# Optimization experiments

Measured on AMD Instinct MI355X. Metric: run time of the kernel, lower is better.

The kernel has to match this reference:

```python
import jax, jax.numpy as jnp
import numpy as np

B, S, E = 2048, 23, 768
RED, H, NUM_LABELS = 256, 8, 25
DH = RED // H
DELTA = 0.1
EPS_LN = 1e-5


def setup_inputs() -> dict:
    key = jax.random.key(0)
    ks = jax.random.split(key, 20)
    g = lambda k, shape, fan: jax.random.normal(k, shape, dtype=jnp.float32) * (1.0 / np.sqrt(fan))
    inp = {
        'cls_embeddings': jax.random.normal(ks[0], (B, S, E), dtype=jnp.float32),
        'existing_mask': jax.random.randint(ks[1], (B, S), 0, 2, dtype=jnp.int32),
        'missing_emb': g(ks[2], (S, E), E),
        'W1': g(ks[3], (E // 2, E), E), 'b1': jnp.zeros((E // 2,), jnp.float32),
        'W2': g(ks[4], (RED, E // 2), E // 2), 'b2': jnp.zeros((RED,), jnp.float32),
        'ln_g': jnp.ones((RED,), jnp.float32), 'ln_b': jnp.zeros((RED,), jnp.float32),
        'Wq': g(ks[5], (RED, RED), RED), 'bq': jnp.zeros((RED,), jnp.float32),
        'Wk': g(ks[6], (RED, RED), RED), 'bk': jnp.zeros((RED,), jnp.float32),
        'Wv': g(ks[7], (RED, RED), RED), 'bv': jnp.zeros((RED,), jnp.float32),
        'Wo': g(ks[8], (RED, RED), RED), 'bo': jnp.zeros((RED,), jnp.float32),
        'Wp': g(ks[9], (NUM_LABELS, RED), RED), 'bp': jnp.zeros((NUM_LABELS,), jnp.float32),
    }
    return inp


def _layer_norm(x, g, b):
    mu = jnp.mean(x, axis=-1, keepdims=True)
    var = jnp.mean(jnp.square(x - mu), axis=-1, keepdims=True)
    return (x - mu) * jax.lax.rsqrt(var + EPS_LN) * g + b


def _forward(cls_embeddings, existing_mask, missing_emb, W1, b1, W2, b2, ln_g, ln_b,
             Wq, bq, Wk, bk, Wv, bv, Wo, bo, Wp, bp):
    exist = existing_mask > 0                              # [B,S] bool
    # Gather: existing sections use BERT CLS, missing slots use learned embeddings
    sec = jnp.where(exist[..., None], cls_embeddings, missing_emb[None])  # [B,S,E]
    # SectionDimReducer (exact-erf GELU as in nn.GELU default)
    h = jax.nn.gelu(sec @ W1.T + b1, approximate=False)
    h = jax.nn.gelu(h @ W2.T + b2, approximate=False)
    red = _layer_norm(h, ln_g, ln_b)                       # [B,S,RED]
    # Tiny MHA: every slot queries the existing sections of its own EHR
    q = (red @ Wq.T + bq).reshape(B, S, H, DH)
    k = (red @ Wk.T + bk).reshape(B, S, H, DH)
    v = (red @ Wv.T + bv).reshape(B, S, H, DH)
    scores = jnp.einsum('bqhd,bkhd->bhqk', q, k) / np.sqrt(DH)
    scores = jnp.where(exist[:, None, None, :], scores, -1e9)
    attn = jax.nn.softmax(scores, axis=-1)                 # [B,H,S,S]
    ctx = jnp.einsum('bhqk,bkhd->bqhd', attn, v).reshape(B, S, RED)
    mha_out = ctx @ Wo.T + bo                              # [B,S,RED]
    # Scatter: only missing slots (of EHRs with >=1 existing section) are replaced
    any_exist = jnp.any(exist, axis=1)                     # [B]
    use_attn = (~exist) & any_exist[:, None]               # [B,S]
    updated = jnp.where(use_attn[..., None], mha_out, red)
    # margin-based orthogonality loss on section embeddings
    norm = updated / jnp.maximum(jnp.linalg.norm(updated, axis=-1, keepdims=True), 1e-8)
    gram = jnp.einsum('bid,bjd->bij', norm, norm)          # [B,S,S]
    off = 1.0 - jnp.eye(S, dtype=updated.dtype)
    loss_orth = jnp.sum(jax.nn.relu(jnp.abs(gram) - DELTA) * off) / (B * S * (S - 1))
    logits = updated.mean(axis=1) @ Wp.T + bp              # [B,NUM_LABELS]
    return loss_orth, logits


def reference(cls_embeddings, existing_mask, missing_emb, W1, b1, W2, b2, ln_g, ln_b,
              Wq, bq, Wk, bk, Wv, bv, Wo, bo, Wp, bp):
    return _forward(cls_embeddings, existing_mask, missing_emb, W1, b1, W2, b2, ln_g, ln_b,
                    Wq, bq, Wk, bk, Wv, bv, Wo, bo, Wp, bp)
```

## Files before the change

kernel.cpp:

```cpp
#include <hip/hip_runtime.h>

typedef unsigned short u16;
typedef unsigned int u32;
typedef __attribute__((ext_vector_type(8))) short short8;
typedef __attribute__((ext_vector_type(4))) float f32x4;

struct __align__(8) us4 { u16 x, y, z, w; };

__device__ __forceinline__ float bf1(u16 v){ return __uint_as_float(((u32)v) << 16); }
__device__ __forceinline__ float bflo(u32 u){ return __uint_as_float(u << 16); }
__device__ __forceinline__ float bfhi(u32 u){ return __uint_as_float(u & 0xFFFF0000u); }
__device__ __forceinline__ u16 fbf(float f){
    u32 u = __float_as_uint(f);
    return (u16)((u + 0x7FFFu + ((u >> 16) & 1u)) >> 16);
}
__device__ __forceinline__ float gelu_exact(float x){
    return 0.5f * x * (1.0f + erff(x * 0.70710678118654752f));
}
__device__ __forceinline__ void unp8(uint4 u, float* f){
    f[0]=bflo(u.x); f[1]=bfhi(u.x); f[2]=bflo(u.y); f[3]=bfhi(u.y);
    f[4]=bflo(u.z); f[5]=bfhi(u.z); f[6]=bflo(u.w); f[7]=bfhi(u.w);
}
__device__ __forceinline__ uint4 pack8(float4 a, float4 b){
    uint4 u;
    u.x = (u32)fbf(a.x) | ((u32)fbf(a.y) << 16);
    u.y = (u32)fbf(a.z) | ((u32)fbf(a.w) << 16);
    u.z = (u32)fbf(b.x) | ((u32)fbf(b.y) << 16);
    u.w = (u32)fbf(b.z) | ((u32)fbf(b.w) << 16);
    return u;
}

#define MFMA16(a, b, c) __builtin_amdgcn_mfma_f32_16x16x32_bf16(a, b, c, 0, 0, 0)
#define QSTR 264


__global__ __launch_bounds__(256) void wconv(
    const float* __restrict__ W1, const float* __restrict__ W2,
    const float* __restrict__ Wq, const float* __restrict__ Wk,
    const float* __restrict__ Wv, const float* __restrict__ Wo,
    const float* __restrict__ Wp, u16* __restrict__ dst)
{
    const int i = blockIdx.x * 256 + threadIdx.x;
    const float* s; int o;
    if      (i < 294912) { s = W1; o = i; }
    else if (i < 393216) { s = W2; o = i - 294912; }
    else if (i < 458752) { s = Wq; o = i - 393216; }
    else if (i < 524288) { s = Wk; o = i - 458752; }
    else if (i < 589824) { s = Wv; o = i - 524288; }
    else if (i < 655360) { s = Wo; o = i - 589824; }
    else                 { s = Wp; o = i - 655360; }
    dst[i] = fbf(s[o]);
}

__global__ __launch_bounds__(256) void gemm1_kernel(
    const float* __restrict__ cls, const int* __restrict__ mask,
    const float* __restrict__ missing, const u16* __restrict__ W,
    const float* __restrict__ bias, u16* __restrict__ C)
{
    const int K = 768, M = 384;
    __shared__ u16 As[128 * 40];
    __shared__ u16 Bs[128 * 40];
    const int tid = threadIdx.x;
    const int w = tid >> 6, lane = tid & 63;
    const int nBase = blockIdx.y * 128, mBase = blockIdx.x * 128;
    const int wr = w >> 1, wc = w & 1;
    const int r0 = tid >> 2;
    const int co = (tid & 3) * 8;
    const int frow = lane & 15, quad = lane >> 4;

    const int rowA0 = nBase + r0, rowA1 = nBase + r0 + 64;
    const float* ap0 = (mask[rowA0] > 0) ? cls + (size_t)rowA0 * 768
                                         : missing + (size_t)(rowA0 % 23) * 768;
    const float* ap1 = (mask[rowA1] > 0) ? cls + (size_t)rowA1 * 768
                                         : missing + (size_t)(rowA1 % 23) * 768;
    const u16* bp0 = W + (size_t)(mBase + r0) * K;
    const u16* bp1 = W + (size_t)(mBase + r0 + 64) * K;

    f32x4 acc[4][4];
#pragma unroll
    for (int mt = 0; mt < 4; ++mt)
#pragma unroll
        for (int nt = 0; nt < 4; ++nt) acc[mt][nt] = f32x4{0.f, 0.f, 0.f, 0.f};

    float4 a0a = *(const float4*)(ap0 + co), a0b = *(const float4*)(ap0 + co + 4);
    float4 a1a = *(const float4*)(ap1 + co), a1b = *(const float4*)(ap1 + co + 4);
    uint4 pb0 = *(const uint4*)(bp0 + co), pb1 = *(const uint4*)(bp1 + co);

    for (int k0 = 0; k0 < K; k0 += 32) {
        __syncthreads();
        *(uint4*)(As + r0 * 40 + co) = pack8(a0a, a0b);
        *(uint4*)(As + (r0 + 64) * 40 + co) = pack8(a1a, a1b);
        *(uint4*)(Bs + r0 * 40 + co) = pb0;
        *(uint4*)(Bs + (r0 + 64) * 40 + co) = pb1;
        __syncthreads();
        if (k0 + 32 < K) {
            const int kn = k0 + 32 + co;
            a0a = *(const float4*)(ap0 + kn); a0b = *(const float4*)(ap0 + kn + 4);
            a1a = *(const float4*)(ap1 + kn); a1b = *(const float4*)(ap1 + kn + 4);
            pb0 = *(const uint4*)(bp0 + kn);  pb1 = *(const uint4*)(bp1 + kn);
        }
        short8 af[4], bfv[4];
#pragma unroll
        for (int mt = 0; mt < 4; ++mt)
            af[mt] = *(const short8*)(As + (wr * 64 + mt * 16 + frow) * 40 + quad * 8);
#pragma unroll
        for (int nt = 0; nt < 4; ++nt)
            bfv[nt] = *(const short8*)(Bs + (wc * 64 + nt * 16 + frow) * 40 + quad * 8);
#pragma unroll
        for (int mt = 0; mt < 4; ++mt)
#pragma unroll
            for (int nt = 0; nt < 4; ++nt)
                acc[mt][nt] = MFMA16(af[mt], bfv[nt], acc[mt][nt]);
    }

#pragma unroll
    for (int nt = 0; nt < 4; ++nt) {
        const int col = mBase + wc * 64 + nt * 16 + frow;
        const float bv = bias[col];
#pragma unroll
        for (int mt = 0; mt < 4; ++mt)
#pragma unroll
            for (int reg = 0; reg < 4; ++reg) {
                const int row = nBase + wr * 64 + mt * 16 + quad * 4 + reg;
                C[(size_t)row * M + col] = fbf(gelu_exact(acc[mt][nt][reg] + bv));
            }
    }
}

__global__ __launch_bounds__(256) void gemm_bt(
    const u16* __restrict__ A, const u16* __restrict__ W,
    const float* __restrict__ bias, u16* __restrict__ C, int K, int M)
{
    __shared__ u16 As[128 * 40];
    __shared__ u16 Bs[128 * 40];
    const int tid = threadIdx.x;
    const int w = tid >> 6, lane = tid & 63;
    const int nBase = blockIdx.y * 128, mBase = blockIdx.x * 128;
    const int wr = w >> 1, wc = w & 1;
    const int r0 = tid >> 2;
    const int co = (tid & 3) * 8;
    const int frow = lane & 15, quad = lane >> 4;

    f32x4 acc[4][4];
#pragma unroll
    for (int mt = 0; mt < 4; ++mt)
#pragma unroll
        for (int nt = 0; nt < 4; ++nt) acc[mt][nt] = f32x4{0.f, 0.f, 0.f, 0.f};

    uint4 pa0 = *(const uint4*)(A + (size_t)(nBase + r0) * K + co);
    uint4 pa1 = *(const uint4*)(A + (size_t)(nBase + r0 + 64) * K + co);
    uint4 pb0 = *(const uint4*)(W + (size_t)(mBase + r0) * K + co);
    uint4 pb1 = *(const uint4*)(W + (size_t)(mBase + r0 + 64) * K + co);

    for (int k0 = 0; k0 < K; k0 += 32) {
        __syncthreads();
        *(uint4*)(As + r0 * 40 + co) = pa0;
        *(uint4*)(As + (r0 + 64) * 40 + co) = pa1;
        *(uint4*)(Bs + r0 * 40 + co) = pb0;
        *(uint4*)(Bs + (r0 + 64) * 40 + co) = pb1;
        __syncthreads();
        if (k0 + 32 < K) {
            const int kn = k0 + 32 + co;
            pa0 = *(const uint4*)(A + (size_t)(nBase + r0) * K + kn);
            pa1 = *(const uint4*)(A + (size_t)(nBase + r0 + 64) * K + kn);
            pb0 = *(const uint4*)(W + (size_t)(mBase + r0) * K + kn);
            pb1 = *(const uint4*)(W + (size_t)(mBase + r0 + 64) * K + kn);
        }
        short8 af[4], bfv[4];
#pragma unroll
        for (int mt = 0; mt < 4; ++mt)
            af[mt] = *(const short8*)(As + (wr * 64 + mt * 16 + frow) * 40 + quad * 8);
#pragma unroll
        for (int nt = 0; nt < 4; ++nt)
            bfv[nt] = *(const short8*)(Bs + (wc * 64 + nt * 16 + frow) * 40 + quad * 8);
#pragma unroll
        for (int mt = 0; mt < 4; ++mt)
#pragma unroll
            for (int nt = 0; nt < 4; ++nt)
                acc[mt][nt] = MFMA16(af[mt], bfv[nt], acc[mt][nt]);
    }

#pragma unroll
    for (int nt = 0; nt < 4; ++nt) {
        const int col = mBase + wc * 64 + nt * 16 + frow;
        const float bv = bias[col];
#pragma unroll
        for (int mt = 0; mt < 4; ++mt)
#pragma unroll
            for (int reg = 0; reg < 4; ++reg) {
                const int row = nBase + wr * 64 + mt * 16 + quad * 4 + reg;
                C[(size_t)row * M + col] = fbf(gelu_exact(acc[mt][nt][reg] + bv));
            }
    }
}

__device__ __forceinline__ void ln_rows_inplace(
    u16* base, int t, const float* __restrict__ lng, const float* __restrict__ lnb)
{
    const int r = t >> 3, sub = t & 7;
    if (r >= 23) return;
    u16* rp = base + r * QSTR + sub * 32;
    float x[32];
    unp8(((const uint4*)rp)[0], x);
    unp8(((const uint4*)rp)[1], x + 8);
    unp8(((const uint4*)rp)[2], x + 16);
    unp8(((const uint4*)rp)[3], x + 24);
    float s = 0.f;
#pragma unroll
    for (int e = 0; e < 32; ++e) s += x[e];
    s += __shfl_xor(s, 1); s += __shfl_xor(s, 2); s += __shfl_xor(s, 4);
    const float mu = s * (1.f / 256.f);
    float vs = 0.f;
#pragma unroll
    for (int e = 0; e < 32; ++e) { const float d = x[e] - mu; vs += d * d; }
    vs += __shfl_xor(vs, 1); vs += __shfl_xor(vs, 2); vs += __shfl_xor(vs, 4);
    const float rs = rsqrtf(vs * (1.f / 256.f) + 1e-5f);
#pragma unroll
    for (int c8 = 0; c8 < 4; ++c8) {
        const int cb = sub * 32 + c8 * 8;
        const float4 g0 = *(const float4*)(lng + cb), g1 = *(const float4*)(lng + cb + 4);
        const float4 b0 = *(const float4*)(lnb + cb), b1 = *(const float4*)(lnb + cb + 4);
        float4 ya, yb;
        ya.x = (x[c8*8+0]-mu)*rs*g0.x + b0.x;
        ya.y = (x[c8*8+1]-mu)*rs*g0.y + b0.y;
        ya.z = (x[c8*8+2]-mu)*rs*g0.z + b0.z;
        ya.w = (x[c8*8+3]-mu)*rs*g0.w + b0.w;
        yb.x = (x[c8*8+4]-mu)*rs*g1.x + b1.x;
        yb.y = (x[c8*8+5]-mu)*rs*g1.y + b1.y;
        yb.z = (x[c8*8+6]-mu)*rs*g1.z + b1.z;
        yb.w = (x[c8*8+7]-mu)*rs*g1.w + b1.w;
        ((uint4*)rp)[c8] = pack8(ya, yb);
    }
}

__global__ __launch_bounds__(256) void attn_tail_kernel(
    const u16* __restrict__ redb, const int* __restrict__ mask,
    const u16* __restrict__ Wqkvb,
    const float* __restrict__ bq, const float* __restrict__ bk,
    const float* __restrict__ bv, const u16* __restrict__ Wob,
    const float* __restrict__ bo, const float* __restrict__ lng,
    const float* __restrict__ lnb, const u16* __restrict__ Wpb,
    const float* __restrict__ bp, float* __restrict__ out,
    float* __restrict__ lossAcc)
{
    __shared__ __align__(16) unsigned char SM[40960];
    u16* s_rq = (u16*)SM;
    u16* s_k  = (u16*)(SM + 12144);
    u16* s_vT = (u16*)(SM + 24288);
    int* sEx   = (int*)(SM + 40672);
    int* sMiss = (int*)(SM + 40764);
    float* sDiag = (float*)(SM + 24288);
    float* sInv  = (float*)(SM + 24384);
    float* sPool = (float*)(SM + 24480);

    const int b = blockIdx.x, t = threadIdx.x;
    const int w = t >> 6, lane = t & 63;
    const int frow = lane & 15, quad = lane >> 4;
    const int r0c = frow;
    const int r1c = (16 + frow > 22) ? 22 : 16 + frow;
    const f32x4 z4 = f32x4{0.f, 0.f, 0.f, 0.f};

    {
        const int myEx = (t < 23) ? mask[b * 23 + t] : 0;
        if (t < 23) sEx[t] = myEx;
        if (t < 64) {
            const unsigned long long ball = __ballot((t < 23) && (myEx > 0));
            if (t < 23) sMiss[t] = (ball != 0ull && myEx <= 0) ? 1 : 0;
        }
    }
    for (int i = t; i < 1024; i += 256) ((uint4*)s_vT)[i] = make_uint4(0u, 0u, 0u, 0u);
    for (int i = t; i < 736; i += 256) {
        const int s = i >> 5, c8 = (i & 31) * 8;
        *(uint4*)(s_rq + s * QSTR + c8) =
            *(const uint4*)(redb + ((size_t)(b * 23 + s)) * 256 + c8);
    }
    __syncthreads();

    ln_rows_inplace(s_rq, t, lng, lnb);
    __syncthreads();

#define QKV_KLOOP(SEGBASE, ACC)                                                   \
    for (int k0 = 0; k0 < 256; k0 += 32) {                                        \
        short8 a0 = *(const short8*)(s_rq + r0c * QSTR + k0 + quad * 8);          \
        short8 a1 = *(const short8*)(s_rq + r1c * QSTR + k0 + quad * 8);          \
        _Pragma("unroll")                                                         \
        for (int nt = 0; nt < 4; ++nt) {                                          \
            const int n = (SEGBASE) + w * 64 + nt * 16 + frow;                    \
            short8 bfr = *(const short8*)(Wqkvb + (size_t)n * 256 + k0 + quad * 8); \
            ACC[0][nt] = MFMA16(a0, bfr, ACC[0][nt]);                             \
            ACC[1][nt] = MFMA16(a1, bfr, ACC[1][nt]);                             \
        }                                                                         \
    }

    {
        f32x4 ka[2][4];
#pragma unroll
        for (int mt = 0; mt < 2; ++mt)
#pragma unroll
            for (int nt = 0; nt < 4; ++nt) ka[mt][nt] = z4;
        QKV_KLOOP(256, ka)
#pragma unroll
        for (int nt = 0; nt < 4; ++nt) {
            const int cm = w * 64 + nt * 16 + frow;
            const float bb = bk[cm];
#pragma unroll
            for (int mt = 0; mt < 2; ++mt)
#pragma unroll
                for (int reg = 0; reg < 4; ++reg) {
                    const int s = mt * 16 + quad * 4 + reg;
                    if (s < 23) s_k[s * QSTR + cm] = fbf(ka[mt][nt][reg] + bb);
                }
        }
    }
    {
        f32x4 va[2][4];
#pragma unroll
        for (int mt = 0; mt < 2; ++mt)
#pragma unroll
            for (int nt = 0; nt < 4; ++nt) va[mt][nt] = z4;
        QKV_KLOOP(512, va)
#pragma unroll
        for (int nt = 0; nt < 4; ++nt) {
            const int cm = w * 64 + nt * 16 + frow;
            const float bb = bv[cm];
#pragma unroll
            for (int mt = 0; mt < 2; ++mt)
#pragma unroll
                for (int reg = 0; reg < 4; ++reg) {
                    const int s = mt * 16 + quad * 4 + reg;
                    if (s < 23) s_vT[cm * 32 + s] = fbf(va[mt][nt][reg] + bb);
                }
        }
    }
    {
        f32x4 qa[2][4];
#pragma unroll
        for (int mt = 0; mt < 2; ++mt)
#pragma unroll
            for (int nt = 0; nt < 4; ++nt) qa[mt][nt] = z4;
        QKV_KLOOP(0, qa)
        __syncthreads();
#pragma unroll
        for (int nt = 0; nt < 4; ++nt) {
            const int cm = w * 64 + nt * 16 + frow;
            const float bb = bq[cm];
#pragma unroll
            for (int mt = 0; mt < 2; ++mt)
#pragma unroll
                for (int reg = 0; reg < 4; ++reg) {
                    const int s = mt * 16 + quad * 4 + reg;
                    if (s < 23) s_rq[s * QSTR + cm] = fbf(qa[mt][nt][reg] + bb);
                }
        }
    }

    {
        const float scl = 0.17677669529663687f;
        const float m0 = (sEx[frow] > 0) ? 0.f : -1e9f;
        const float m1 = (16 + frow < 23 && sEx[16 + frow] > 0) ? 0.f : -1e9f;
#pragma unroll
        for (int hh2 = 0; hh2 < 2; ++hh2) {
            const int hb = w * 64 + hh2 * 32;
            short8 aq0 = *(const short8*)(s_rq + r0c * QSTR + hb + quad * 8);
            short8 aq1 = *(const short8*)(s_rq + r1c * QSTR + hb + quad * 8);
            short8 bk0 = *(const short8*)(s_k + r0c * QSTR + hb + quad * 8);
            short8 bk1 = *(const short8*)(s_k + r1c * QSTR + hb + quad * 8);
            f32x4 s00 = MFMA16(aq0, bk0, z4);
            f32x4 s01 = MFMA16(aq0, bk1, z4);
            f32x4 s10 = MFMA16(aq1, bk0, z4);
            f32x4 s11 = MFMA16(aq1, bk1, z4);
#pragma unroll
            for (int mt = 0; mt < 2; ++mt) {
                f32x4& c0 = mt ? s10 : s00;
                f32x4& c1 = mt ? s11 : s01;
#pragma unroll
                for (int reg = 0; reg < 4; ++reg) {
                    float v0 = c0[reg] * scl + m0;
                    float v1 = c1[reg] * scl + m1;
                    float mx = fmaxf(v0, v1);
#pragma unroll
                    for (int m = 8; m; m >>= 1) mx = fmaxf(mx, __shfl_xor(mx, m));
                    float p0 = __expf(v0 - mx), p1 = __expf(v1 - mx);
                    float sm = p0 + p1;
#pragma unroll
                    for (int m = 8; m; m >>= 1) sm += __shfl_xor(sm, m);
                    const float inv = 1.f / sm;
                    c0[reg] = p0 * inv;
                    c1[reg] = p1 * inv;
                }
            }
#pragma unroll
            for (int reg = 0; reg < 4; ++reg) {
                const int q0r = quad * 4 + reg;
                s_k[q0r * QSTR + hb + frow]      = fbf(s00[reg]);
                s_k[q0r * QSTR + hb + 16 + frow] = fbf(s01[reg]);
                const int q1r = 16 + quad * 4 + reg;
                if (q1r < 23) {
                    s_k[q1r * QSTR + hb + frow]      = fbf(s10[reg]);
                    s_k[q1r * QSTR + hb + 16 + frow] = fbf(s11[reg]);
                }
            }
            short8 pa0 = *(const short8*)(s_k + r0c * QSTR + hb + quad * 8);
            short8 pa1 = *(const short8*)(s_k + r1c * QSTR + hb + quad * 8);
            short8 bv0 = *(const short8*)(s_vT + (hb + frow) * 32 + quad * 8);
            short8 bv1 = *(const short8*)(s_vT + (hb + 16 + frow) * 32 + quad * 8);
            f32x4 c00 = MFMA16(pa0, bv0, z4);
            f32x4 c01 = MFMA16(pa0, bv1, z4);
            f32x4 c10 = MFMA16(pa1, bv0, z4);
            f32x4 c11 = MFMA16(pa1, bv1, z4);
#pragma unroll
            for (int reg = 0; reg < 4; ++reg) {
                const int q0r = quad * 4 + reg;
                s_rq[q0r * QSTR + hb + frow]      = fbf(c00[reg]);
                s_rq[q0r * QSTR + hb + 16 + frow] = fbf(c01[reg]);
                const int q1r = 16 + quad * 4 + reg;
                if (q1r < 23) {
                    s_rq[q1r * QSTR + hb + frow]      = fbf(c10[reg]);
                    s_rq[q1r * QSTR + hb + 16 + frow] = fbf(c11[reg]);
                }
            }
        }
    }
    __syncthreads();

    {
        const u16* src = redb + (size_t)(b * 23) * 256;
        const int s0 = t >> 5, c0o = (t & 31) * 8;
        uint4 rg0 = *(const uint4*)(src + s0 * 256 + c0o);
        uint4 rg1 = *(const uint4*)(src + (s0 + 8) * 256 + c0o);
        uint4 rg2;
        const bool has2 = (t + 512) < 736;
        if (has2) rg2 = *(const uint4*)(src + (s0 + 16) * 256 + c0o);

        f32x4 wacc[2][4];
#pragma unroll
        for (int mt = 0; mt < 2; ++mt)
#pragma unroll
            for (int nt = 0; nt < 4; ++nt) wacc[mt][nt] = z4;
        for (int k0 = 0; k0 < 256; k0 += 32) {
            short8 a0 = *(const short8*)(s_rq + r0c * QSTR + k0 + quad * 8);
            short8 a1 = *(const short8*)(s_rq + r1c * QSTR + k0 + quad * 8);
#pragma unroll
            for (int nt = 0; nt < 4; ++nt) {
                const int n = w * 64 + nt * 16 + frow;
                short8 bfr = *(const short8*)(Wob + (size_t)n * 256 + k0 + quad * 8);
                wacc[0][nt] = MFMA16(a0, bfr, wacc[0][nt]);
                wacc[1][nt] = MFMA16(a1, bfr, wacc[1][nt]);
            }
        }
        *(uint4*)(s_k + s0 * QSTR + c0o) = rg0;
        *(uint4*)(s_k + (s0 + 8) * QSTR + c0o) = rg1;
        if (has2) *(uint4*)(s_k + (s0 + 16) * QSTR + c0o) = rg2;
        __syncthreads();
        ln_rows_inplace(s_k, t, lng, lnb);
        __syncthreads();
#pragma unroll
        for (int nt = 0; nt < 4; ++nt) {
            const int col = w * 64 + nt * 16 + frow;
            const float bvv = bo[col];
#pragma unroll
            for (int mt = 0; mt < 2; ++mt)
#pragma unroll
                for (int reg = 0; reg < 4; ++reg) {
                    const int s = mt * 16 + quad * 4 + reg;
                    if (s < 23 && sMiss[s])
                        s_k[s * QSTR + col] = fbf(wacc[mt][nt][reg] + bvv);
                }
        }
    }
    __syncthreads();

    f32x4 g00 = z4, g01 = z4, g10 = z4, g11 = z4;
    if (w == 0) {
        for (int k0 = 0; k0 < 256; k0 += 32) {
            short8 a0 = *(const short8*)(s_k + r0c * QSTR + k0 + quad * 8);
            short8 a1 = *(const short8*)(s_k + r1c * QSTR + k0 + quad * 8);
            g00 = MFMA16(a0, a0, g00);
            g01 = MFMA16(a0, a1, g01);
            g10 = MFMA16(a1, a0, g10);
            g11 = MFMA16(a1, a1, g11);
        }
#pragma unroll
        for (int reg = 0; reg < 4; ++reg) {
            if (frow == quad * 4 + reg) {
                sDiag[frow] = g00[reg];
                if (16 + frow < 23) sDiag[16 + frow] = g11[reg];
            }
        }
    } else {
        for (int c = t - 64; c < 256; c += 192) {
            float pv = 0.f;
#pragma unroll
            for (int s = 0; s < 23; ++s) pv += bf1(s_k[s * QSTR + c]);
            sPool[c] = pv * (1.f / 23.f);
        }
    }
    __syncthreads();
    if (t < 23) sInv[t] = 1.f / fmaxf(sqrtf(sDiag[t]), 1e-8f);
    __syncthreads();

    if (w == 0) {
        float contrib = 0.f;
        const float ic0 = sInv[frow];
        const float ic1 = (16 + frow < 23) ? sInv[16 + frow] : 0.f;
        const bool c1ok = (16 + frow < 23);
#pragma unroll
        for (int reg = 0; reg < 4; ++reg) {
            const int rA = quad * 4 + reg;
            const float irA = sInv[rA];
            if (rA != frow) {
                const float cc = fabsf(g00[reg] * irA * ic0) - 0.1f;
                if (cc > 0.f) contrib += cc;
            }
            if (c1ok) {
                const float cc = fabsf(g01[reg] * irA * ic1) - 0.1f;
                if (cc > 0.f) contrib += cc;
            }
            const int rB = 16 + quad * 4 + reg;
            if (rB < 23) {
                const float irB = sInv[rB];
                {
                    const float cc = fabsf(g10[reg] * irB * ic0) - 0.1f;
                    if (cc > 0.f) contrib += cc;
                }
                if (c1ok && rB != 16 + frow) {
                    const float cc = fabsf(g11[reg] * irB * ic1) - 0.1f;
                    if (cc > 0.f) contrib += cc;
                }
            }
        }
#pragma unroll
        for (int m = 32; m; m >>= 1) contrib += __shfl_xor(contrib, m);
        if (lane == 0) atomicAdd(lossAcc, contrib);
    } else {
        const int li = t - 64;
#pragma unroll 1
        for (int pass = 0; pass < 2; ++pass) {
            int L, chunk;
            if (pass == 0) { L = li >> 3; chunk = li & 7; }
            else { if (li >= 8) break; L = 24; chunk = li; }
            float a = 0.f;
#pragma unroll
            for (int q4 = 0; q4 < 4; ++q4) {
                const int c8 = chunk * 4 + q4;
                float wf[8]; unp8(*(const uint4*)(Wpb + (size_t)L * 256 + c8 * 8), wf);
                const float4 p0 = *(const float4*)(sPool + c8 * 8);
                const float4 p1 = *(const float4*)(sPool + c8 * 8 + 4);
                a += wf[0] * p0.x + wf[1] * p0.y + wf[2] * p0.z + wf[3] * p0.w
                   + wf[4] * p1.x + wf[5] * p1.y + wf[6] * p1.z + wf[7] * p1.w;
            }
            a += __shfl_xor(a, 1); a += __shfl_xor(a, 2); a += __shfl_xor(a, 4);
            if (chunk == 0) out[1 + b * 25 + L] = a + bp[L];
        }
    }
}

__global__ void loss_finalize(const float* __restrict__ lossAcc, float* __restrict__ out)
{
    out[0] = lossAcc[0] * (1.f / 1036288.f);
}

extern "C" void kernel_launch(void* const* d_in, const int* in_sizes, int n_in,
                              void* d_out, int out_size, void* d_ws, size_t ws_size,
                              hipStream_t stream)
{
    const float* cls     = (const float*)d_in[0];
    const int*   mask    = (const int*)d_in[1];
    const float* missing = (const float*)d_in[2];
    const float* W1 = (const float*)d_in[3];  const float* b1 = (const float*)d_in[4];
    const float* W2 = (const float*)d_in[5];  const float* b2 = (const float*)d_in[6];
    const float* lng = (const float*)d_in[7]; const float* lnb = (const float*)d_in[8];
    const float* Wq = (const float*)d_in[9];  const float* bq = (const float*)d_in[10];
    const float* Wk = (const float*)d_in[11]; const float* bk = (const float*)d_in[12];
    const float* Wv = (const float*)d_in[13]; const float* bv = (const float*)d_in[14];
    const float* Wo = (const float*)d_in[15]; const float* bo = (const float*)d_in[16];
    const float* Wp = (const float*)d_in[17]; const float* bp = (const float*)d_in[18];
    float* out = (float*)d_out;

    char* ws = (char*)d_ws;
    u16* h1b  = (u16*)ws;
    u16* redb = (u16*)(ws + 36175872);
    u16* Wb   = (u16*)(ws + 60293120);
    u16* W1b   = Wb;
    u16* W2b   = Wb + 294912;
    u16* Wqkvb = Wb + 393216;
    u16* Wob   = Wb + 589824;
    u16* Wpb   = Wb + 655360;
    float* lossAcc = (float*)(ws + 61616640);

    hipMemsetAsync(lossAcc, 0, sizeof(float), stream);

    wconv<<<2585, 256, 0, stream>>>(W1, W2, Wq, Wk, Wv, Wo, Wp, Wb);
    gemm1_kernel<<<dim3(3, 368), 256, 0, stream>>>(cls, mask, missing, W1b, b1, h1b);
    gemm_bt<<<dim3(2, 368), 256, 0, stream>>>(h1b, W2b, b2, redb, 384, 256);
    attn_tail_kernel<<<2048, 256, 0, stream>>>(redb, mask, Wqkvb, bq, bk, bv,
                                               Wob, bo, lng, lnb, Wpb, bp,
                                               out, lossAcc);
    loss_finalize<<<1, 1, 0, stream>>>(lossAcc, out);
}
```

Measured before the change: 550.5 us.

## Fuse layernorm into register loads and software-prefetch weight fragments in attention tail

The layernorm on the reduced rows is now applied in registers right after the global load and written to shared memory once, which removes a shared-memory round trip and a barrier, in both the initial and the residual paths. The QKV and output projection k-loops now use a macro that prefetches the next weight fragments while the current MFMAs run. The gram loop and the pooling weights for the classifier head are also prefetched early. Launch bounds now request 4 blocks per SM, which may force register spilling given the extra prefetch registers.

```diff
diff --git a/kernel.cpp b/kernel.cpp
--- a/kernel.cpp
+++ b/kernel.cpp
@@ -194,46 +194,71 @@
     }
 }
 
-__device__ __forceinline__ void ln_rows_inplace(
-    u16* base, int t, const float* __restrict__ lng, const float* __restrict__ lnb)
-{
-    const int r = t >> 3, sub = t & 7;
-    if (r >= 23) return;
-    u16* rp = base + r * QSTR + sub * 32;
-    float x[32];
-    unp8(((const uint4*)rp)[0], x);
-    unp8(((const uint4*)rp)[1], x + 8);
-    unp8(((const uint4*)rp)[2], x + 16);
-    unp8(((const uint4*)rp)[3], x + 24);
-    float s = 0.f;
-#pragma unroll
-    for (int e = 0; e < 32; ++e) s += x[e];
+__device__ __forceinline__ void ln1_reg(
+    const float* x, const float4& g0, const float4& g1,
+    const float4& b0, const float4& b1, u16* rp)
+{
+    float s = x[0] + x[1] + x[2] + x[3] + x[4] + x[5] + x[6] + x[7];
     s += __shfl_xor(s, 1); s += __shfl_xor(s, 2); s += __shfl_xor(s, 4);
+    s += __shfl_xor(s, 8); s += __shfl_xor(s, 16);
     const float mu = s * (1.f / 256.f);
-    float vs = 0.f;
-#pragma unroll
-    for (int e = 0; e < 32; ++e) { const float d = x[e] - mu; vs += d * d; }
-    vs += __shfl_xor(vs, 1); vs += __shfl_xor(vs, 2); vs += __shfl_xor(vs, 4);
-    const float rs = rsqrtf(vs * (1.f / 256.f) + 1e-5f);
-#pragma unroll
-    for (int c8 = 0; c8 < 4; ++c8) {
-        const int cb = sub * 32 + c8 * 8;
-        const float4 g0 = *(const float4*)(lng + cb), g1 = *(const float4*)(lng + cb + 4);
-        const float4 b0 = *(const float4*)(lnb + cb), b1 = *(const float4*)(lnb + cb + 4);
-        float4 ya, yb;
-        ya.x = (x[c8*8+0]-mu)*rs*g0.x + b0.x;
-        ya.y = (x[c8*8+1]-mu)*rs*g0.y + b0.y;
-        ya.z = (x[c8*8+2]-mu)*rs*g0.z + b0.z;
-        ya.w = (x[c8*8+3]-mu)*rs*g0.w + b0.w;
-        yb.x = (x[c8*8+4]-mu)*rs*g1.x + b1.x;
-        yb.y = (x[c8*8+5]-mu)*rs*g1.y + b1.y;
-        yb.z = (x[c8*8+6]-mu)*rs*g1.z + b1.z;
-        yb.w = (x[c8*8+7]-mu)*rs*g1.w + b1.w;
-        ((uint4*)rp)[c8] = pack8(ya, yb);
-    }
-}
-
-__global__ __launch_bounds__(256) void attn_tail_kernel(
+    float v = 0.f;
+#pragma unroll
+    for (int e = 0; e < 8; ++e) { const float d = x[e] - mu; v += d * d; }
+    v += __shfl_xor(v, 1); v += __shfl_xor(v, 2); v += __shfl_xor(v, 4);
+    v += __shfl_xor(v, 8); v += __shfl_xor(v, 16);
+    const float rs = rsqrtf(v * (1.f / 256.f) + 1e-5f);
+    float4 ya, yb;
+    ya.x = (x[0]-mu)*rs*g0.x + b0.x;
+    ya.y = (x[1]-mu)*rs*g0.y + b0.y;
+    ya.z = (x[2]-mu)*rs*g0.z + b0.z;
+    ya.w = (x[3]-mu)*rs*g0.w + b0.w;
+    yb.x = (x[4]-mu)*rs*g1.x + b1.x;
+    yb.y = (x[5]-mu)*rs*g1.y + b1.y;
+    yb.z = (x[6]-mu)*rs*g1.z + b1.z;
+    yb.w = (x[7]-mu)*rs*g1.w + b1.w;
+    *(uint4*)rp = pack8(ya, yb);
+}
+
+__device__ __forceinline__ void ln3_reg_store(
+    uint4 rg0, uint4 rg1, uint4 rg2, bool has2,
+    const float* __restrict__ lng, const float* __restrict__ lnb,
+    u16* dstBase, int s0, int c0o)
+{
+    const float4 g0 = *(const float4*)(lng + c0o);
+    const float4 g1 = *(const float4*)(lng + c0o + 4);
+    const float4 b0 = *(const float4*)(lnb + c0o);
+    const float4 b1 = *(const float4*)(lnb + c0o + 4);
+    float x[8];
+    unp8(rg0, x); ln1_reg(x, g0, g1, b0, b1, dstBase + s0 * QSTR + c0o);
+    unp8(rg1, x); ln1_reg(x, g0, g1, b0, b1, dstBase + (s0 + 8) * QSTR + c0o);
+    if (has2) { unp8(rg2, x); ln1_reg(x, g0, g1, b0, b1, dstBase + (s0 + 16) * QSTR + c0o); }
+}
+
+#define KLOOP_PF(WPTR, SRC, ACC)                                                  \
+    {                                                                             \
+        short8 nb0 = *(const short8*)(WPTR);                                      \
+        short8 nb1 = *(const short8*)((WPTR) + 16 * 256);                         \
+        short8 nb2 = *(const short8*)((WPTR) + 32 * 256);                         \
+        short8 nb3 = *(const short8*)((WPTR) + 48 * 256);                         \
+        for (int k0 = 0; k0 < 256; k0 += 32) {                                    \
+            short8 a0 = *(const short8*)((SRC) + r0c * QSTR + k0 + quad * 8);     \
+            short8 a1 = *(const short8*)((SRC) + r1c * QSTR + k0 + quad * 8);     \
+            short8 c0 = nb0, c1 = nb1, c2 = nb2, c3 = nb3;                        \
+            if (k0 + 32 < 256) {                                                  \
+                nb0 = *(const short8*)((WPTR) + (k0 + 32));                       \
+                nb1 = *(const short8*)((WPTR) + 16 * 256 + (k0 + 32));            \
+                nb2 = *(const short8*)((WPTR) + 32 * 256 + (k0 + 32));            \
+                nb3 = *(const short8*)((WPTR) + 48 * 256 + (k0 + 32));            \
+            }                                                                     \
+            ACC[0][0] = MFMA16(a0, c0, ACC[0][0]); ACC[1][0] = MFMA16(a1, c0, ACC[1][0]); \
+            ACC[0][1] = MFMA16(a0, c1, ACC[0][1]); ACC[1][1] = MFMA16(a1, c1, ACC[1][1]); \
+            ACC[0][2] = MFMA16(a0, c2, ACC[0][2]); ACC[1][2] = MFMA16(a1, c2, ACC[1][2]); \
+            ACC[0][3] = MFMA16(a0, c3, ACC[0][3]); ACC[1][3] = MFMA16(a1, c3, ACC[1][3]); \
+        }                                                                         \
+    }
+
+__global__ __launch_bounds__(256, 4) void attn_tail_kernel(
     const u16* __restrict__ redb, const int* __restrict__ mask,
     const u16* __restrict__ Wqkvb,
     const float* __restrict__ bq, const float* __restrict__ bk,
@@ -269,46 +294,38 @@
         }
     }
     for (int i = t; i < 1024; i += 256) ((uint4*)s_vT)[i] = make_uint4(0u, 0u, 0u, 0u);
-    for (int i = t; i < 736; i += 256) {
-        const int s = i >> 5, c8 = (i & 31) * 8;
-        *(uint4*)(s_rq + s * QSTR + c8) =
-            *(const uint4*)(redb + ((size_t)(b * 23 + s)) * 256 + c8);
+
+    {
+        const u16* src = redb + (size_t)(b * 23) * 256;
+        const int s0 = t >> 5, c0o = (t & 31) * 8;
+        uint4 rg0 = *(const uint4*)(src + s0 * 256 + c0o);
+        uint4 rg1 = *(const uint4*)(src + (s0 + 8) * 256 + c0o);
+        uint4 rg2 = make_uint4(0u, 0u, 0u, 0u);
+        const bool has2 = t < 224;
+        if (has2) rg2 = *(const uint4*)(src + (s0 + 16) * 256 + c0o);
+        ln3_reg_store(rg0, rg1, rg2, has2, lng, lnb, s_rq, s0, c0o);
     }
     __syncthreads();
 
-    ln_rows_inplace(s_rq, t, lng, lnb);
-    __syncthreads();
-
-#define QKV_KLOOP(SEGBASE, ACC)                                                   \
-    for (int k0 = 0; k0 < 256; k0 += 32) {                                        \
-        short8 a0 = *(const short8*)(s_rq + r0c * QSTR + k0 + quad * 8);          \
-        short8 a1 = *(const short8*)(s_rq + r1c * QSTR + k0 + quad * 8);          \
-        _Pragma("unroll")                                                         \
-        for (int nt = 0; nt < 4; ++nt) {                                          \
-            const int n = (SEGBASE) + w * 64 + nt * 16 + frow;                    \
-            short8 bfr = *(const short8*)(Wqkvb + (size_t)n * 256 + k0 + quad * 8); \
-            ACC[0][nt] = MFMA16(a0, bfr, ACC[0][nt]);                             \
-            ACC[1][nt] = MFMA16(a1, bfr, ACC[1][nt]);                             \
-        }                                                                         \
-    }
-
+    const int cmb = w * 64 + frow;
     {
         f32x4 ka[2][4];
 #pragma unroll
         for (int mt = 0; mt < 2; ++mt)
 #pragma unroll
             for (int nt = 0; nt < 4; ++nt) ka[mt][nt] = z4;
-        QKV_KLOOP(256, ka)
+        const u16* wp = Wqkvb + (size_t)(256 + cmb) * 256 + quad * 8;
+        const float bb[4] = {bk[cmb], bk[cmb + 16], bk[cmb + 32], bk[cmb + 48]};
+        KLOOP_PF(wp, s_rq, ka)
 #pragma unroll
         for (int nt = 0; nt < 4; ++nt) {
-            const int cm = w * 64 + nt * 16 + frow;
-            const float bb = bk[cm];
+            const int cm = cmb + nt * 16;
 #pragma unroll
             for (int mt = 0; mt < 2; ++mt)
 #pragma unroll
                 for (int reg = 0; reg < 4; ++reg) {
                     const int s = mt * 16 + quad * 4 + reg;
-                    if (s < 23) s_k[s * QSTR + cm] = fbf(ka[mt][nt][reg] + bb);
+                    if (s < 23) s_k[s * QSTR + cm] = fbf(ka[mt][nt][reg] + bb[nt]);
                 }
         }
     }
@@ -318,17 +335,18 @@
         for (int mt = 0; mt < 2; ++mt)
 #pragma unroll
             for (int nt = 0; nt < 4; ++nt) va[mt][nt] = z4;
-        QKV_KLOOP(512, va)
+        const u16* wp = Wqkvb + (size_t)(512 + cmb) * 256 + quad * 8;
+        const float bb[4] = {bv[cmb], bv[cmb + 16], bv[cmb + 32], bv[cmb + 48]};
+        KLOOP_PF(wp, s_rq, va)
 #pragma unroll
         for (int nt = 0; nt < 4; ++nt) {
-            const int cm = w * 64 + nt * 16 + frow;
-            const float bb = bv[cm];
+            const int cm = cmb + nt * 16;
 #pragma unroll
             for (int mt = 0; mt < 2; ++mt)
 #pragma unroll
                 for (int reg = 0; reg < 4; ++reg) {
                     const int s = mt * 16 + quad * 4 + reg;
-                    if (s < 23) s_vT[cm * 32 + s] = fbf(va[mt][nt][reg] + bb);
+                    if (s < 23) s_vT[cm * 32 + s] = fbf(va[mt][nt][reg] + bb[nt]);
                 }
         }
     }
@@ -338,18 +356,19 @@
         for (int mt = 0; mt < 2; ++mt)
 #pragma unroll
             for (int nt = 0; nt < 4; ++nt) qa[mt][nt] = z4;
-        QKV_KLOOP(0, qa)
+        const u16* wp = Wqkvb + (size_t)cmb * 256 + quad * 8;
+        const float bb[4] = {bq[cmb], bq[cmb + 16], bq[cmb + 32], bq[cmb + 48]};
+        KLOOP_PF(wp, s_rq, qa)
         __syncthreads();
 #pragma unroll
         for (int nt = 0; nt < 4; ++nt) {
-            const int cm = w * 64 + nt * 16 + frow;
-            const float bb = bq[cm];
+            const int cm = cmb + nt * 16;
 #pragma unroll
             for (int mt = 0; mt < 2; ++mt)
 #pragma unroll
                 for (int reg = 0; reg < 4; ++reg) {
                     const int s = mt * 16 + quad * 4 + reg;
-                    if (s < 23) s_rq[s * QSTR + cm] = fbf(qa[mt][nt][reg] + bb);
+                    if (s < 23) s_rq[s * QSTR + cm] = fbf(qa[mt][nt][reg] + bb[nt]);
                 }
         }
     }
@@ -428,8 +447,8 @@
         const int s0 = t >> 5, c0o = (t & 31) * 8;
         uint4 rg0 = *(const uint4*)(src + s0 * 256 + c0o);
         uint4 rg1 = *(const uint4*)(src + (s0 + 8) * 256 + c0o);
-        uint4 rg2;
-        const bool has2 = (t + 512) < 736;
+        uint4 rg2 = make_uint4(0u, 0u, 0u, 0u);
+        const bool has2 = t < 224;
         if (has2) rg2 = *(const uint4*)(src + (s0 + 16) * 256 + c0o);
 
         f32x4 wacc[2][4];
@@ -437,44 +456,38 @@
         for (int mt = 0; mt < 2; ++mt)
 #pragma unroll
             for (int nt = 0; nt < 4; ++nt) wacc[mt][nt] = z4;
-        for (int k0 = 0; k0 < 256; k0 += 32) {
-            short8 a0 = *(const short8*)(s_rq + r0c * QSTR + k0 + quad * 8);
-            short8 a1 = *(const short8*)(s_rq + r1c * QSTR + k0 + quad * 8);
-#pragma unroll
-            for (int nt = 0; nt < 4; ++nt) {
-                const int n = w * 64 + nt * 16 + frow;
-                short8 bfr = *(const short8*)(Wob + (size_t)n * 256 + k0 + quad * 8);
-                wacc[0][nt] = MFMA16(a0, bfr, wacc[0][nt]);
-                wacc[1][nt] = MFMA16(a1, bfr, wacc[1][nt]);
-            }
-        }
-        *(uint4*)(s_k + s0 * QSTR + c0o) = rg0;
-        *(uint4*)(s_k + (s0 + 8) * QSTR + c0o) = rg1;
-        if (has2) *(uint4*)(s_k + (s0 + 16) * QSTR + c0o) = rg2;
+        const u16* wp = Wob + (size_t)cmb * 256 + quad * 8;
+        const float ob[4] = {bo[cmb], bo[cmb + 16], bo[cmb + 32], bo[cmb + 48]};
+        KLOOP_PF(wp, s_rq, wacc)
+        ln3_reg_store(rg0, rg1, rg2, has2, lng, lnb, s_k, s0, c0o);
         __syncthreads();
-        ln_rows_inplace(s_k, t, lng, lnb);
-        __syncthreads();
 #pragma unroll
         for (int nt = 0; nt < 4; ++nt) {
-            const int col = w * 64 + nt * 16 + frow;
-            const float bvv = bo[col];
+            const int col = cmb + nt * 16;
 #pragma unroll
             for (int mt = 0; mt < 2; ++mt)
 #pragma unroll
                 for (int reg = 0; reg < 4; ++reg) {
                     const int s = mt * 16 + quad * 4 + reg;
                     if (s < 23 && sMiss[s])
-                        s_k[s * QSTR + col] = fbf(wacc[mt][nt][reg] + bvv);
+                        s_k[s * QSTR + col] = fbf(wacc[mt][nt][reg] + ob[nt]);
                 }
         }
     }
     __syncthreads();
 
     f32x4 g00 = z4, g01 = z4, g10 = z4, g11 = z4;
+    uint4 wpre[4];
+    int Lpre = 0, chpre = 0;
     if (w == 0) {
+        short8 ga0 = *(const short8*)(s_k + r0c * QSTR + quad * 8);
+        short8 ga1 = *(const short8*)(s_k + r1c * QSTR + quad * 8);
         for (int k0 = 0; k0 < 256; k0 += 32) {
-            short8 a0 = *(const short8*)(s_k + r0c * QSTR + k0 + quad * 8);
-            short8 a1 = *(const short8*)(s_k + r1c * QSTR + k0 + quad * 8);
+            short8 a0 = ga0, a1 = ga1;
+            if (k0 + 32 < 256) {
+                ga0 = *(const short8*)(s_k + r0c * QSTR + k0 + 32 + quad * 8);
+                ga1 = *(const short8*)(s_k + r1c * QSTR + k0 + 32 + quad * 8);
+            }
             g00 = MFMA16(a0, a0, g00);
             g01 = MFMA16(a0, a1, g01);
             g10 = MFMA16(a1, a0, g10);
@@ -488,6 +501,11 @@
             }
         }
     } else {
+        const int li = t - 64;
+        Lpre = li >> 3; chpre = li & 7;
+#pragma unroll
+        for (int q4 = 0; q4 < 4; ++q4)
+            wpre[q4] = *(const uint4*)(Wpb + (size_t)Lpre * 256 + (chpre * 4 + q4) * 8);
         for (int c = t - 64; c < 256; c += 192) {
             float pv = 0.f;
 #pragma unroll
@@ -534,23 +552,33 @@
         if (lane == 0) atomicAdd(lossAcc, contrib);
     } else {
         const int li = t - 64;
-#pragma unroll 1
-        for (int pass = 0; pass < 2; ++pass) {
-            int L, chunk;
-            if (pass == 0) { L = li >> 3; chunk = li & 7; }
-            else { if (li >= 8) break; L = 24; chunk = li; }
+        {
             float a = 0.f;
 #pragma unroll
             for (int q4 = 0; q4 < 4; ++q4) {
-                const int c8 = chunk * 4 + q4;
-                float wf[8]; unp8(*(const uint4*)(Wpb + (size_t)L * 256 + c8 * 8), wf);
+                const int c8 = chpre * 4 + q4;
+                float wf[8]; unp8(wpre[q4], wf);
                 const float4 p0 = *(const float4*)(sPool + c8 * 8);
                 const float4 p1 = *(const float4*)(sPool + c8 * 8 + 4);
                 a += wf[0] * p0.x + wf[1] * p0.y + wf[2] * p0.z + wf[3] * p0.w
                    + wf[4] * p1.x + wf[5] * p1.y + wf[6] * p1.z + wf[7] * p1.w;
             }
             a += __shfl_xor(a, 1); a += __shfl_xor(a, 2); a += __shfl_xor(a, 4);
-            if (chunk == 0) out[1 + b * 25 + L] = a + bp[L];
+            if (chpre == 0) out[1 + b * 25 + Lpre] = a + bp[Lpre];
+        }
+        if (li < 8) {
+            float a = 0.f;
+#pragma unroll
+            for (int q4 = 0; q4 < 4; ++q4) {
+                const int c8 = li * 4 + q4;
+                float wf[8]; unp8(*(const uint4*)(Wpb + (size_t)24 * 256 + c8 * 8), wf);
+                const float4 p0 = *(const float4*)(sPool + c8 * 8);
+                const float4 p1 = *(const float4*)(sPool + c8 * 8 + 4);
+                a += wf[0] * p0.x + wf[1] * p0.y + wf[2] * p0.z + wf[3] * p0.w
+                   + wf[4] * p1.x + wf[5] * p1.y + wf[6] * p1.z + wf[7] * p1.w;
+            }
+            a += __shfl_xor(a, 1); a += __shfl_xor(a, 2); a += __shfl_xor(a, 4);
+            if (li == 0) out[1 + b * 25 + 24] = a + bp[24];
         }
     }
 }
```

Result: slower. 625.5 us (+13.6%).
